# Optimization experiments

Measured on AMD Instinct MI355X. Metric: run time of the kernel, lower is better.

The kernel has to match this reference:

```python
import jax, jax.numpy as jnp
import numpy as np

LN_EPS = 1e-5

def _layernorm(x, g, b):
    mu = jnp.mean(x, axis=-1, keepdims=True)
    var = jnp.mean(jnp.square(x - mu), axis=-1, keepdims=True)
    return (x - mu) * jax.lax.rsqrt(var + LN_EPS) * g + b

def setup_inputs() -> dict:
    key = jax.random.key(0)
    ks = jax.random.split(key, 12)
    B, S, E = 8, 4096, 512
    H, DK = 64, 8          # d_k = E // H = 8 qubits per head
    NQ_FFN, FFN = 8, 2048
    TWO_PI = 2.0 * np.pi
    x = jax.random.normal(ks[0], (B, S, E), dtype=jnp.float32)
    # trainable RX phases per attention head/wire; trainable RY phases for FFN qubits
    theta_attn = jax.random.uniform(ks[1], (H, DK), dtype=jnp.float32, maxval=TWO_PI)
    theta_ffn = jax.random.uniform(ks[2], (NQ_FFN,), dtype=jnp.float32, maxval=TWO_PI)
    s_e = 1.0 / np.sqrt(E)
    W_comb = jax.random.uniform(ks[3], (E, E), dtype=jnp.float32, minval=-s_e, maxval=s_e)
    b_comb = jax.random.uniform(ks[4], (E,), dtype=jnp.float32, minval=-s_e, maxval=s_e)
    s_q = 1.0 / np.sqrt(NQ_FFN)
    W1 = jax.random.uniform(ks[5], (FFN, NQ_FFN), dtype=jnp.float32, minval=-s_q, maxval=s_q)
    b1 = jax.random.uniform(ks[6], (FFN,), dtype=jnp.float32, minval=-s_q, maxval=s_q)
    s_f = 1.0 / np.sqrt(FFN)
    W2 = jax.random.uniform(ks[7], (E, FFN), dtype=jnp.float32, minval=-s_f, maxval=s_f)
    b2 = jax.random.uniform(ks[8], (E,), dtype=jnp.float32, minval=-s_f, maxval=s_f)
    ln1_g = jnp.ones((E,), jnp.float32); ln1_b = jnp.zeros((E,), jnp.float32)
    ln2_g = jnp.ones((E,), jnp.float32); ln2_b = jnp.zeros((E,), jnp.float32)
    return {"x": x, "theta_attn": theta_attn, "W_comb": W_comb, "b_comb": b_comb,
            "ln1_g": ln1_g, "ln1_b": ln1_b, "theta_ffn": theta_ffn,
            "W1": W1, "b1": b1, "W2": W2, "b2": b2, "ln2_g": ln2_g, "ln2_b": ln2_b}

def reference(x, theta_attn, W_comb, b_comb, ln1_g, ln1_b, theta_ffn, W1, b1, W2, b2, ln2_g, ln2_b):
    B, S, E = x.shape
    H, DK = theta_attn.shape
    NQ = theta_ffn.shape[0]
    # Quantum attention heads: RX(x) then RX(theta) on |0> per wire -> <Z> = cos(x+theta)
    q = jnp.cos(x.reshape(B, S, H, DK) + theta_attn)  # [B,S,H,DK]
    attn_out = jnp.einsum('bse,fe->bsf', q.reshape(B, S, E), W_comb) + b_comb
    x1 = _layernorm(x + attn_out, ln1_g, ln1_b)
    # Quantum FFN layer: RY(x) then RY(theta) -> <Z> = cos(x+theta), first NQ features only
    fq = jnp.cos(x1[..., :NQ] + theta_ffn)            # [B,S,NQ]
    h = jax.nn.relu(jnp.einsum('bsq,fq->bsf', fq, W1) + b1)
    ffn_out = jnp.einsum('bsf,ef->bse', h, W2) + b2
    return _layernorm(x1 + ffn_out, ln2_g, ln2_b)
```

## Files before the change

kernel.cpp:

```cpp
#include <hip/hip_runtime.h>
#include <stdint.h>

typedef unsigned short u16;
typedef __bf16 bf16x8 __attribute__((ext_vector_type(8)));
typedef float f32x4 __attribute__((ext_vector_type(4)));

#define AS1(p) ((const __attribute__((address_space(1))) void*)(p))
#define AS3(p) ((__attribute__((address_space(3))) void*)(p))

__device__ __forceinline__ float b2f(u16 v){
    union { unsigned u; float f; } x; x.u = ((unsigned)v) << 16; return x.f;
}
__device__ __forceinline__ u16 f2b(float f){
    union { float f; unsigned u; } x; x.f = f;
    unsigned r = x.u + 0x7FFFu + ((x.u >> 16) & 1u);
    return (u16)(r >> 16);
}

__global__ __launch_bounds__(256) void probe_kernel(
    const u16* p0,const u16* p1,const u16* p2,const u16* p3,const u16* p4,
    const u16* p5,const u16* p6,const u16* p7,const u16* p8,const u16* p9,
    const u16* p10,const u16* p11,const u16* p12,
    int n0,int n1,int n2,int n3,int n4,int n5,int n6,int n7,int n8,int n9,
    int n10,int n11,int n12, int* flags)
{
    const u16* p; int n;
    switch (blockIdx.x) {
        case 0: p=p0; n=n0; break;   case 1: p=p1; n=n1; break;
        case 2: p=p2; n=n2; break;   case 3: p=p3; n=n3; break;
        case 4: p=p4; n=n4; break;   case 5: p=p5; n=n5; break;
        case 6: p=p6; n=n6; break;   case 7: p=p7; n=n7; break;
        case 8: p=p8; n=n8; break;   case 9: p=p9; n=n9; break;
        case 10: p=p10; n=n10; break; case 11: p=p11; n=n11; break;
        default: p=p12; n=n12; break;
    }
    int pairs = n >> 1; if (pairs > 2048) pairs = 2048;
    int strong = 0, znz = 0, tot = 0;
    for (int k = threadIdx.x; k < pairs; k += 256) {
        u16 lo = p[2*k], hi = p[2*k+1];
        int eh = (hi >> 7) & 0xFF;
        int el = (lo >> 7) & 0xFF;
        if (eh >= 0xF0 || (eh >= 1 && eh <= 0x40)) strong = 1;
        if (el >= 0xF0 || (el >= 1 && el <= 0x40)) strong = 1;
        if (lo == 0 && hi != 0) znz++;
        tot++;
    }
    __shared__ int ss, sz, st;
    if (threadIdx.x == 0) { ss = 0; sz = 0; st = 0; }
    __syncthreads();
    if (strong) atomicOr(&ss, 1);
    if (znz) atomicAdd(&sz, znz);
    atomicAdd(&st, tot);
    __syncthreads();
    if (threadIdx.x == 0) {
        flags[blockIdx.x] = (ss || (2 * sz > st)) ? 1 : 0;
        if (blockIdx.x == 0) flags[15] = 0;
    }
}

__global__ __launch_bounds__(256) void convert_kernel(
    const void* sWc, const void* sW2, const void* sW1,
    const void* sTa, const void* sBc, const void* sG1, const void* sB1l,
    const void* sTf, const void* sB1, const void* sB2, const void* sG2, const void* sB2l,
    u16* wbase, const int* flags)
{
    int b = blockIdx.x;
    const void* src; u16* dst; int n, fi, lb, tof32 = 0;
    if (b < 128)      { src=sWc; dst=wbase;          n=262144;  fi=2;  lb=b; }
    else if (b < 640) { src=sW2; dst=wbase+262144;   n=1048576; fi=9;  lb=b-128; }
    else if (b >= 643 && b < 651) { src=sW1; dst=wbase+1312256; n=16384; fi=7; lb=b-643; }
    else {
        lb = 0;
        switch (b) {
            case 640: src=sTa;  dst=wbase+1310720; n=512;  fi=1;  break;
            case 641: src=sBc;  dst=wbase+1311232; n=512;  fi=3;  break;
            case 642: src=sB2;  dst=wbase+1311744; n=512;  fi=10; break;
            case 651: src=sB1;  dst=wbase+1328640; n=2048; fi=8;  break;
            case 652: src=sG1;  dst=wbase+1330688; n=512;  fi=4;  break;
            case 653: src=sB1l; dst=wbase+1331200; n=512;  fi=5;  break;
            case 654: src=sG2;  dst=wbase+1331712; n=512;  fi=11; break;
            case 655: src=sB2l; dst=wbase+1332224; n=512;  fi=12; break;
            default:  src=sTf;  dst=wbase+1332736; n=8;    fi=6;  tof32=1; break;
        }
    }
    int i = lb * 256 + threadIdx.x;
    if (i * 8 >= n) return;
    if (tof32) {
        float* fd = (float*)dst;
        if (flags[fi]) {
            const float4* s = (const float4*)src;
            ((float4*)fd)[i*2] = s[i*2]; ((float4*)fd)[i*2+1] = s[i*2+1];
        } else {
            union { uint4 v; u16 h[8]; } sb;
            sb.v = ((const uint4*)src)[i];
            #pragma unroll
            for (int j = 0; j < 8; j++) fd[i*8+j] = b2f(sb.h[j]);
        }
        return;
    }
    if (flags[fi]) {
        const float4* s = (const float4*)src;
        float4 a = s[i*2], c = s[i*2+1];
        union { uint4 v; u16 h[8]; } o;
        o.h[0]=f2b(a.x); o.h[1]=f2b(a.y); o.h[2]=f2b(a.z); o.h[3]=f2b(a.w);
        o.h[4]=f2b(c.x); o.h[5]=f2b(c.y); o.h[6]=f2b(c.z); o.h[7]=f2b(c.w);
        ((uint4*)dst)[i] = o.v;
    } else {
        ((uint4*)dst)[i] = ((const uint4*)src)[i];
    }
}

__global__ __launch_bounds__(256) void qgen_kernel(
    const void* __restrict__ x, const u16* __restrict__ theta,
    u16* __restrict__ q, const int* flags)
{
    const int idx = blockIdx.x * 256 + threadIdx.x;
    const int col0 = (idx * 8) & 511;
    union { uint4 v; u16 h[8]; } tb;
    tb.v = *(const uint4*)(theta + col0);
    float xv[8];
    if (flags[0]) {
        const float4* p = (const float4*)x + idx * 2;
        float4 a = p[0], b = p[1];
        xv[0]=a.x; xv[1]=a.y; xv[2]=a.z; xv[3]=a.w;
        xv[4]=b.x; xv[5]=b.y; xv[6]=b.z; xv[7]=b.w;
    } else {
        union { uint4 v; u16 h[8]; } xb;
        xb.v = ((const uint4*)x)[idx];
        #pragma unroll
        for (int e = 0; e < 8; e++) xv[e] = b2f(xb.h[e]);
    }
    union { uint4 v; u16 h[8]; } o;
    #pragma unroll
    for (int e = 0; e < 8; e++) o.h[e] = f2b(__cosf(xv[e] + b2f(tb.h[e])));
    ((uint4*)q)[idx] = o.v;
}

__global__ __launch_bounds__(512, 2) void gemm1_fused(
    const u16* q, const void* __restrict__ x,
    const u16* __restrict__ Wt, const u16* __restrict__ bias,
    const u16* __restrict__ g1, const u16* __restrict__ b1l,
    const float* __restrict__ tf,
    u16* x1out, u16* __restrict__ fqout, const int* flags)
{
    __shared__ __align__(16) u16 As[2][128 * 64];
    __shared__ __align__(16) u16 Bs[2][512 * 64];
    const int K = 512, N = 512;
    const int tid  = threadIdx.x;
    const int lane = tid & 63;
    const int w    = tid >> 6;

    const int m0 = blockIdx.x * 128;

    const int srow = lane >> 3;
    const int scol = ((lane & 7) ^ srow) * 8;
    const int wm = (w >> 2) * 64;
    const int wn = (w & 3) * 128;
    const int fr   = lane & 15;
    const int quad = lane >> 4;
    const int fx   = fr & 7;
    const int isf32 = flags[0];

    f32x4 acc[4][8];
    #pragma unroll
    for (int i = 0; i < 4; i++)
        #pragma unroll
        for (int jj = 0; jj < 8; jj++)
            acc[i][jj] = f32x4{0.f, 0.f, 0.f, 0.f};

    const u16* Abase = q  + (size_t)m0 * K + scol;
    const u16* Bbase = Wt + scol;

    #pragma unroll
    for (int i = 0; i < 2; i++) {
        int c = w * 2 + i;
        int row = c * 8 + srow;
        __builtin_amdgcn_global_load_lds(AS1(Abase + (size_t)row * K),
                                         AS3(&As[0][c * 512]), 16, 0, 0);
    }
    #pragma unroll
    for (int i = 0; i < 8; i++) {
        int c = w * 8 + i;
        int row = c * 8 + srow;
        __builtin_amdgcn_global_load_lds(AS1(Bbase + (size_t)row * K),
                                         AS3(&Bs[0][c * 512]), 16, 0, 0);
    }

    int cur = 0;
    for (int kt = 0; kt < K; kt += 64) {
        __syncthreads();
        if (kt + 64 < K) {
            int nxt = cur ^ 1;
            #pragma unroll
            for (int i = 0; i < 2; i++) {
                int c = w * 2 + i;
                int row = c * 8 + srow;
                __builtin_amdgcn_global_load_lds(
                    AS1(Abase + (size_t)row * K + kt + 64),
                    AS3(&As[nxt][c * 512]), 16, 0, 0);
            }
            #pragma unroll
            for (int i = 0; i < 8; i++) {
                int c = w * 8 + i;
                int row = c * 8 + srow;
                __builtin_amdgcn_global_load_lds(
                    AS1(Bbase + (size_t)row * K + kt + 64),
                    AS3(&Bs[nxt][c * 512]), 16, 0, 0);
            }
        }
        #pragma unroll
        for (int kk = 0; kk < 2; kk++) {
            bf16x8 af[4];
            #pragma unroll
            for (int mi = 0; mi < 4; mi++)
                af[mi] = *(const bf16x8*)(&As[cur][(wm + mi * 16 + fr) * 64 +
                                          (((kk * 4 + quad) ^ fx) * 8)]);
            #pragma unroll
            for (int np = 0; np < 4; np++) {
                bf16x8 bfr[2];
                #pragma unroll
                for (int ni = 0; ni < 2; ni++)
                    bfr[ni] = *(const bf16x8*)(&Bs[cur][(wn + (np * 2 + ni) * 16 + fr) * 64 +
                                               (((kk * 4 + quad) ^ fx) * 8)]);
                #pragma unroll
                for (int mi = 0; mi < 4; mi++)
                    #pragma unroll
                    for (int ni = 0; ni < 2; ni++)
                        acc[mi][np * 2 + ni] = __builtin_amdgcn_mfma_f32_16x16x32_bf16(
                            af[mi], bfr[ni], acc[mi][np * 2 + ni], 0, 0, 0);
            }
        }
        cur ^= 1;
    }

    __syncthreads();
    u16* zt = &Bs[0][0];
    #pragma unroll
    for (int mi = 0; mi < 4; mi++) {
        #pragma unroll
        for (int nq = 0; nq < 8; nq++) {
            int n = wn + nq * 16 + fr;
            float bn = b2f(bias[n]);
            #pragma unroll
            for (int r = 0; r < 4; r++) {
                int lm = wm + mi * 16 + quad * 4 + r;
                float rv = isf32 ? ((const float*)x)[(size_t)(m0 + lm) * N + n]
                                 : b2f(((const u16*)x)[(size_t)(m0 + lm) * N + n]);
                zt[lm * 512 + n] = f2b(acc[mi][nq][r] + bn + rv);
            }
        }
    }
    __syncthreads();

    {
        union { uint4 v; u16 s[8]; } gb, bb;
        gb.v = *(const uint4*)(g1 + lane * 8);
        bb.v = *(const uint4*)(b1l + lane * 8);
        for (int i = 0; i < 16; i++) {
            int row = w * 16 + i;
            union { uint4 v; u16 s[8]; } zb;
            zb.v = ((const uint4*)(zt + row * 512))[lane];
            float xv[8], s = 0.f, ss = 0.f;
            #pragma unroll
            for (int jj = 0; jj < 8; jj++) {
                xv[jj] = b2f(zb.s[jj]); s += xv[jj]; ss += xv[jj] * xv[jj];
            }
            #pragma unroll
            for (int o = 32; o > 0; o >>= 1) { s += __shfl_down(s, o); ss += __shfl_down(ss, o); }
            s = __shfl(s, 0); ss = __shfl(ss, 0);
            float mu = s * (1.f / 512.f);
            float rs = rsqrtf(ss * (1.f / 512.f) - mu * mu + 1e-5f);
            float xn[8];
            union { uint4 v; u16 s[8]; } ob;
            #pragma unroll
            for (int jj = 0; jj < 8; jj++) {
                xn[jj] = (xv[jj] - mu) * rs * b2f(gb.s[jj]) + b2f(bb.s[jj]);
                ob.s[jj] = f2b(xn[jj]);
            }
            ((uint4*)(x1out + (size_t)(m0 + row) * 512))[lane] = ob.v;
            if (lane == 0) {
                #pragma unroll
                for (int jj = 0; jj < 8; jj++)
                    fqout[(size_t)(m0 + row) * 8 + jj] = f2b(__cosf(xn[jj] + tf[jj]));
            }
        }
    }
}

__global__ __launch_bounds__(512, 2) void gemm2_fused(
    const u16* __restrict__ fq, const u16* __restrict__ W1, const u16* __restrict__ b1,
    const u16* __restrict__ Wt, const u16* __restrict__ bias,
    const u16* __restrict__ res, const u16* __restrict__ g2, const u16* __restrict__ b2l,
    void* __restrict__ out, const int* flags)
{
    __shared__ __align__(16) u16 Bs[2][512 * 64];
    const int K = 2048, N = 512;
    const int tid  = threadIdx.x;
    const int lane = tid & 63;
    const int w    = tid >> 6;

    const int m0 = blockIdx.x * 128;

    const int srow = lane >> 3;
    const int scol = ((lane & 7) ^ srow) * 8;
    const int wm = (w >> 2) * 64;
    const int wn = (w & 3) * 128;
    const int fr   = lane & 15;
    const int quad = lane >> 4;
    const int fx   = fr & 7;
    const int isf32 = flags[0];

    bf16x8 fqf[4];
    #pragma unroll
    for (int mi = 0; mi < 4; mi++) {
        union { uint4 v; bf16x8 b; } z; z.v = uint4{0,0,0,0};
        if (quad == 0) z.v = *(const uint4*)(fq + (size_t)(m0 + wm + mi * 16 + fr) * 8);
        fqf[mi] = z.b;
    }

    const int krow = ((fr >> 2) * 8) + (fr & 3);

    union { uint4 v; bf16x8 b; } w1f[4];
    uint2 b1f[4];
    #pragma unroll
    for (int g = 0; g < 4; g++) {
        w1f[g].v = uint4{0,0,0,0};
        if (quad == 0)
            w1f[g].v = *(const uint4*)(W1 + (size_t)((g >> 1) * 32 + (g & 1) * 4 + krow) * 8);
        b1f[g] = *(const uint2*)(b1 + (g >> 1) * 32 + (g & 1) * 4 + quad * 8);
    }

    f32x4 acc[4][8];
    #pragma unroll
    for (int i = 0; i < 4; i++)
        #pragma unroll
        for (int jj = 0; jj < 8; jj++)
            acc[i][jj] = f32x4{0.f, 0.f, 0.f, 0.f};

    const u16* Bbase = Wt + scol;
    #pragma unroll
    for (int i = 0; i < 8; i++) {
        int c = w * 8 + i;
        int row = c * 8 + srow;
        __builtin_amdgcn_global_load_lds(AS1(Bbase + (size_t)row * K),
                                         AS3(&Bs[0][c * 512]), 16, 0, 0);
    }

    int cur = 0;
    for (int kt = 0; kt < K; kt += 64) {
        __syncthreads();
        if (kt + 64 < K) {
            int nxt = cur ^ 1;
            #pragma unroll
            for (int i = 0; i < 8; i++) {
                int c = w * 8 + i;
                int row = c * 8 + srow;
                __builtin_amdgcn_global_load_lds(
                    AS1(Bbase + (size_t)row * K + kt + 64),
                    AS3(&Bs[nxt][c * 512]), 16, 0, 0);
            }
        }
        #pragma unroll
        for (int kk = 0; kk < 2; kk++) {
            const u16* pb0 = (const u16*)&b1f[kk * 2 + 0];
            const u16* pb1 = (const u16*)&b1f[kk * 2 + 1];
            f32x4 c0 = {b2f(pb0[0]), b2f(pb0[1]), b2f(pb0[2]), b2f(pb0[3])};
            f32x4 c1 = {b2f(pb1[0]), b2f(pb1[1]), b2f(pb1[2]), b2f(pb1[3])};
            bf16x8 af[4];
            #pragma unroll
            for (int mi = 0; mi < 4; mi++) {
                f32x4 hv0 = __builtin_amdgcn_mfma_f32_16x16x32_bf16(
                    w1f[kk * 2 + 0].b, fqf[mi], c0, 0, 0, 0);
                f32x4 hv1 = __builtin_amdgcn_mfma_f32_16x16x32_bf16(
                    w1f[kk * 2 + 1].b, fqf[mi], c1, 0, 0, 0);
                #pragma unroll
                for (int r = 0; r < 4; r++) {
                    af[mi][r]     = (__bf16)fmaxf(hv0[r], 0.f);
                    af[mi][4 + r] = (__bf16)fmaxf(hv1[r], 0.f);
                }
            }
            #pragma unroll
            for (int np = 0; np < 4; np++) {
                bf16x8 bfr[2];
                #pragma unroll
                for (int ni = 0; ni < 2; ni++)
                    bfr[ni] = *(const bf16x8*)(&Bs[cur][(wn + (np * 2 + ni) * 16 + fr) * 64 +
                                               (((kk * 4 + quad) ^ fx) * 8)]);
                #pragma unroll
                for (int mi = 0; mi < 4; mi++)
                    #pragma unroll
                    for (int ni = 0; ni < 2; ni++)
                        acc[mi][np * 2 + ni] = __builtin_amdgcn_mfma_f32_16x16x32_bf16(
                            af[mi], bfr[ni], acc[mi][np * 2 + ni], 0, 0, 0);
            }
        }
        if (kt + 64 < K) {
            #pragma unroll
            for (int g = 0; g < 4; g++) {
                if (quad == 0)
                    w1f[g].v = *(const uint4*)(W1 +
                        (size_t)(kt + 64 + (g >> 1) * 32 + (g & 1) * 4 + krow) * 8);
                b1f[g] = *(const uint2*)(b1 + kt + 64 + (g >> 1) * 32 + (g & 1) * 4 + quad * 8);
            }
        }
        cur ^= 1;
    }

    __syncthreads();
    u16* zt = &Bs[0][0];
    #pragma unroll
    for (int mi = 0; mi < 4; mi++) {
        #pragma unroll
        for (int nq = 0; nq < 8; nq++) {
            int n = wn + nq * 16 + fr;
            float bn = b2f(bias[n]);
            #pragma unroll
            for (int r = 0; r < 4; r++) {
                int lm = wm + mi * 16 + quad * 4 + r;
                float v = acc[mi][nq][r] + bn + b2f(res[(size_t)(m0 + lm) * N + n]);
                zt[lm * 512 + n] = f2b(v);
            }
        }
    }
    __syncthreads();

    {
        union { uint4 v; u16 s[8]; } gb, bb;
        gb.v = *(const uint4*)(g2 + lane * 8);
        bb.v = *(const uint4*)(b2l + lane * 8);
        for (int i = 0; i < 16; i++) {
            int row = w * 16 + i;
            union { uint4 v; u16 s[8]; } zb;
            zb.v = ((const uint4*)(zt + row * 512))[lane];
            float xv[8], s = 0.f, ss = 0.f;
            #pragma unroll
            for (int jj = 0; jj < 8; jj++) {
                xv[jj] = b2f(zb.s[jj]); s += xv[jj]; ss += xv[jj] * xv[jj];
            }
            #pragma unroll
            for (int o = 32; o > 0; o >>= 1) { s += __shfl_down(s, o); ss += __shfl_down(ss, o); }
            s = __shfl(s, 0); ss = __shfl(ss, 0);
            float mu = s * (1.f / 512.f);
            float rs = rsqrtf(ss * (1.f / 512.f) - mu * mu + 1e-5f);
            size_t m = (size_t)(m0 + row);
            if (isf32) {
                float xn[8];
                #pragma unroll
                for (int jj = 0; jj < 8; jj++)
                    xn[jj] = (xv[jj] - mu) * rs * b2f(gb.s[jj]) + b2f(bb.s[jj]);
                float* po = (float*)out + m * N + lane * 8;
                *(float4*)po       = float4{xn[0], xn[1], xn[2], xn[3]};
                *(float4*)(po + 4) = float4{xn[4], xn[5], xn[6], xn[7]};
            } else {
                union { uint4 v; u16 s[8]; } ob;
                #pragma unroll
                for (int jj = 0; jj < 8; jj++)
                    ob.s[jj] = f2b((xv[jj] - mu) * rs * b2f(gb.s[jj]) + b2f(bb.s[jj]));
                ((uint4*)((u16*)out + m * N))[lane] = ob.v;
            }
        }
    }
}

extern "C" void kernel_launch(void* const* d_in, const int* in_sizes, int n_in,
                              void* d_out, int out_size, void* d_ws, size_t ws_size,
                              hipStream_t stream)
{
    u16* ws16 = (u16*)d_ws;
    u16* W     = ws16;
    int* flags = (int*)(ws16 + 1332752);
    u16* fq  = ws16 + 1332800;
    u16* x1  = ws16 + 1594944;
    u16* q   = x1;

    const u16*  wWc  = W;
    const u16*  wW2  = W + 262144;
    const u16*  wTa  = W + 1310720;
    const u16*  wBc  = W + 1311232;
    const u16*  wB2  = W + 1311744;
    const u16*  wW1  = W + 1312256;
    const u16*  wB1  = W + 1328640;
    const u16*  wG1  = W + 1330688;
    const u16*  wB1l = W + 1331200;
    const u16*  wG2  = W + 1331712;
    const u16*  wB2l = W + 1332224;
    const float* wTf = (const float*)(W + 1332736);

    probe_kernel<<<13, 256, 0, stream>>>(
        (const u16*)d_in[0], (const u16*)d_in[1], (const u16*)d_in[2],
        (const u16*)d_in[3], (const u16*)d_in[4], (const u16*)d_in[5],
        (const u16*)d_in[6], (const u16*)d_in[7], (const u16*)d_in[8],
        (const u16*)d_in[9], (const u16*)d_in[10], (const u16*)d_in[11],
        (const u16*)d_in[12],
        in_sizes[0], in_sizes[1], in_sizes[2], in_sizes[3], in_sizes[4],
        in_sizes[5], in_sizes[6], in_sizes[7], in_sizes[8], in_sizes[9],
        in_sizes[10], in_sizes[11], in_sizes[12], flags);

    convert_kernel<<<657, 256, 0, stream>>>(
        d_in[2], d_in[9], d_in[7], d_in[1], d_in[3], d_in[4], d_in[5],
        d_in[6], d_in[8], d_in[10], d_in[11], d_in[12], (u16*)W, flags);

    qgen_kernel<<<8192, 256, 0, stream>>>(d_in[0], wTa, q, flags);

    gemm1_fused<<<256, 512, 0, stream>>>(
        q, d_in[0], wWc, wBc, wG1, wB1l, wTf, x1, fq, flags);

    gemm2_fused<<<256, 512, 0, stream>>>(
        fq, wW1, wB1, wW2, wB2, x1, wG2, wB2l, d_out, flags);
}
```

Measured before the change: 301.3 us.

## Triple-buffer W2 tiles with K=32 stages and stage W1/b1 in LDS

Restructures the fused FFN GEMM main loop from double-buffered 64-wide K tiles to a three-stage ring of 32-wide K tiles, using explicit vmcnt waits so up to two tile loads stay in flight. W1 and b1 are preloaded into LDS once instead of being re-read from global memory every iteration, and s_setprio is raised around the MFMA section. This aims to hide global-load latency and cut per-iteration global traffic. In exchange there are twice as many barriers per K and LDS use grows to about 132 KB, which may lower occupancy compared with the intended two blocks per CU.

```diff
diff --git a/kernel.cpp b/kernel.cpp
--- a/kernel.cpp
+++ b/kernel.cpp
@@ -293,22 +293,22 @@
     const u16* __restrict__ res, const u16* __restrict__ g2, const u16* __restrict__ b2l,
     void* __restrict__ out, const int* flags)
 {
-    __shared__ __align__(16) u16 Bs[2][512 * 64];
-    const int K = 2048, N = 512;
+    __shared__ __align__(16) u16 pool[67584];
+    const int K = 2048, N = 512, NT = 64;
     const int tid  = threadIdx.x;
     const int lane = tid & 63;
     const int w    = tid >> 6;
 
     const int m0 = blockIdx.x * 128;
 
-    const int srow = lane >> 3;
-    const int scol = ((lane & 7) ^ srow) * 8;
     const int wm = (w >> 2) * 64;
     const int wn = (w & 3) * 128;
     const int fr   = lane & 15;
     const int quad = lane >> 4;
-    const int fx   = fr & 7;
     const int isf32 = flags[0];
+
+    u16* W1lds = pool + 49152;
+    u16* b1lds = pool + 65536;
 
     bf16x8 fqf[4];
     #pragma unroll
@@ -317,18 +317,7 @@
         if (quad == 0) z.v = *(const uint4*)(fq + (size_t)(m0 + wm + mi * 16 + fr) * 8);
         fqf[mi] = z.b;
     }
-
     const int krow = ((fr >> 2) * 8) + (fr & 3);
-
-    union { uint4 v; bf16x8 b; } w1f[4];
-    uint2 b1f[4];
-    #pragma unroll
-    for (int g = 0; g < 4; g++) {
-        w1f[g].v = uint4{0,0,0,0};
-        if (quad == 0)
-            w1f[g].v = *(const uint4*)(W1 + (size_t)((g >> 1) * 32 + (g & 1) * 4 + krow) * 8);
-        b1f[g] = *(const uint2*)(b1 + (g >> 1) * 32 + (g & 1) * 4 + quad * 8);
-    }
 
     f32x4 acc[4][8];
     #pragma unroll
@@ -337,77 +326,97 @@
         for (int jj = 0; jj < 8; jj++)
             acc[i][jj] = f32x4{0.f, 0.f, 0.f, 0.f};
 
-    const u16* Bbase = Wt + scol;
-    #pragma unroll
-    for (int i = 0; i < 8; i++) {
-        int c = w * 8 + i;
-        int row = c * 8 + srow;
-        __builtin_amdgcn_global_load_lds(AS1(Bbase + (size_t)row * K),
-                                         AS3(&Bs[0][c * 512]), 16, 0, 0);
-    }
-
-    int cur = 0;
-    for (int kt = 0; kt < K; kt += 64) {
-        __syncthreads();
-        if (kt + 64 < K) {
-            int nxt = cur ^ 1;
-            #pragma unroll
-            for (int i = 0; i < 8; i++) {
-                int c = w * 8 + i;
-                int row = c * 8 + srow;
-                __builtin_amdgcn_global_load_lds(
-                    AS1(Bbase + (size_t)row * K + kt + 64),
-                    AS3(&Bs[nxt][c * 512]), 16, 0, 0);
-            }
-        }
-        #pragma unroll
-        for (int kk = 0; kk < 2; kk++) {
-            const u16* pb0 = (const u16*)&b1f[kk * 2 + 0];
-            const u16* pb1 = (const u16*)&b1f[kk * 2 + 1];
-            f32x4 c0 = {b2f(pb0[0]), b2f(pb0[1]), b2f(pb0[2]), b2f(pb0[3])};
-            f32x4 c1 = {b2f(pb1[0]), b2f(pb1[1]), b2f(pb1[2]), b2f(pb1[3])};
-            bf16x8 af[4];
-            #pragma unroll
-            for (int mi = 0; mi < 4; mi++) {
-                f32x4 hv0 = __builtin_amdgcn_mfma_f32_16x16x32_bf16(
-                    w1f[kk * 2 + 0].b, fqf[mi], c0, 0, 0, 0);
-                f32x4 hv1 = __builtin_amdgcn_mfma_f32_16x16x32_bf16(
-                    w1f[kk * 2 + 1].b, fqf[mi], c1, 0, 0, 0);
-                #pragma unroll
-                for (int r = 0; r < 4; r++) {
-                    af[mi][r]     = (__bf16)fmaxf(hv0[r], 0.f);
-                    af[mi][4 + r] = (__bf16)fmaxf(hv1[r], 0.f);
-                }
-            }
-            #pragma unroll
-            for (int np = 0; np < 4; np++) {
-                bf16x8 bfr[2];
+    #pragma unroll
+    for (int i = 0; i < 4; i++) {
+        int c = w * 4 + i;
+        __builtin_amdgcn_global_load_lds(AS1(W1 + (size_t)c * 512 + lane * 8),
+                                         AS3(W1lds + c * 512), 16, 0, 0);
+    }
+    if (w < 4)
+        __builtin_amdgcn_global_load_lds(AS1(b1 + (size_t)w * 512 + lane * 8),
+                                         AS3(b1lds + w * 512), 16, 0, 0);
+    const int rr = lane >> 2;
+    const int soct = (lane & 3) ^ (rr & 3);
+    const u16* Bsrc = Wt + (size_t)rr * K + soct * 8;
+    auto STAGE = [&](int tt, int bb) {
+        #pragma unroll
+        for (int i = 0; i < 4; i++) {
+            int c = w * 4 + i;
+            __builtin_amdgcn_global_load_lds(
+                AS1(Bsrc + (size_t)(c * 16) * K + tt * 32),
+                AS3(pool + bb * 16384 + c * 512), 16, 0, 0);
+        }
+    };
+    STAGE(0, 0);
+    STAGE(1, 1);
+    __syncthreads();
+
+    union { uint4 v; bf16x8 b; } w1c0, w1c1;
+    uint2 b1c0, b1c1;
+    w1c0.v = uint4{0,0,0,0}; w1c1.v = uint4{0,0,0,0};
+    if (quad == 0) {
+        w1c0.v = *(const uint4*)(W1lds + (size_t)krow * 8);
+        w1c1.v = *(const uint4*)(W1lds + (size_t)(4 + krow) * 8);
+    }
+    b1c0 = *(const uint2*)(b1lds + quad * 8);
+    b1c1 = *(const uint2*)(b1lds + 4 + quad * 8);
+
+    const int rbase = (wn + fr) * 32 + ((quad ^ (fr & 3)) * 8);
+
+    int bcur = 0, bstage = 2;
+    for (int t = 0; t < NT; ++t) {
+        __builtin_amdgcn_sched_barrier(0);
+        if (t < NT - 1) asm volatile("s_waitcnt vmcnt(4)" ::: "memory");
+        else            asm volatile("s_waitcnt vmcnt(0)" ::: "memory");
+        __builtin_amdgcn_s_barrier();
+        __builtin_amdgcn_sched_barrier(0);
+        if (t + 2 < NT) STAGE(t + 2, bstage);
+
+        const u16* pb0 = (const u16*)&b1c0;
+        const u16* pb1 = (const u16*)&b1c1;
+        f32x4 c0 = {b2f(pb0[0]), b2f(pb0[1]), b2f(pb0[2]), b2f(pb0[3])};
+        f32x4 c1 = {b2f(pb1[0]), b2f(pb1[1]), b2f(pb1[2]), b2f(pb1[3])};
+        bf16x8 af[4];
+        #pragma unroll
+        for (int mi = 0; mi < 4; mi++) {
+            f32x4 hv0 = __builtin_amdgcn_mfma_f32_16x16x32_bf16(w1c0.b, fqf[mi], c0, 0, 0, 0);
+            f32x4 hv1 = __builtin_amdgcn_mfma_f32_16x16x32_bf16(w1c1.b, fqf[mi], c1, 0, 0, 0);
+            #pragma unroll
+            for (int r = 0; r < 4; r++) {
+                af[mi][r]     = (__bf16)fmaxf(hv0[r], 0.f);
+                af[mi][4 + r] = (__bf16)fmaxf(hv1[r], 0.f);
+            }
+        }
+        if (t + 1 < NT) {
+            if (quad == 0) {
+                w1c0.v = *(const uint4*)(W1lds + (size_t)((t + 1) * 32 + krow) * 8);
+                w1c1.v = *(const uint4*)(W1lds + (size_t)((t + 1) * 32 + 4 + krow) * 8);
+            }
+            b1c0 = *(const uint2*)(b1lds + (t + 1) * 32 + quad * 8);
+            b1c1 = *(const uint2*)(b1lds + (t + 1) * 32 + 4 + quad * 8);
+        }
+        const u16* BsBuf = pool + bcur * 16384;
+        __builtin_amdgcn_s_setprio(1);
+        #pragma unroll
+        for (int np = 0; np < 4; np++) {
+            bf16x8 bfr[2];
+            #pragma unroll
+            for (int ni = 0; ni < 2; ni++)
+                bfr[ni] = *(const bf16x8*)(BsBuf + rbase + (np * 2 + ni) * 512);
+            #pragma unroll
+            for (int mi = 0; mi < 4; mi++)
                 #pragma unroll
                 for (int ni = 0; ni < 2; ni++)
-                    bfr[ni] = *(const bf16x8*)(&Bs[cur][(wn + (np * 2 + ni) * 16 + fr) * 64 +
-                                               (((kk * 4 + quad) ^ fx) * 8)]);
-                #pragma unroll
-                for (int mi = 0; mi < 4; mi++)
-                    #pragma unroll
-                    for (int ni = 0; ni < 2; ni++)
-                        acc[mi][np * 2 + ni] = __builtin_amdgcn_mfma_f32_16x16x32_bf16(
-                            af[mi], bfr[ni], acc[mi][np * 2 + ni], 0, 0, 0);
-            }
-        }
-        if (kt + 64 < K) {
-            #pragma unroll
-            for (int g = 0; g < 4; g++) {
-                if (quad == 0)
-                    w1f[g].v = *(const uint4*)(W1 +
-                        (size_t)(kt + 64 + (g >> 1) * 32 + (g & 1) * 4 + krow) * 8);
-                b1f[g] = *(const uint2*)(b1 + kt + 64 + (g >> 1) * 32 + (g & 1) * 4 + quad * 8);
-            }
-        }
-        cur ^= 1;
-    }
-
-    __syncthreads();
-    u16* zt = &Bs[0][0];
+                    acc[mi][np * 2 + ni] = __builtin_amdgcn_mfma_f32_16x16x32_bf16(
+                        af[mi], bfr[ni], acc[mi][np * 2 + ni], 0, 0, 0);
+        }
+        __builtin_amdgcn_s_setprio(0);
+        bcur   = (bcur   == 2) ? 0 : bcur + 1;
+        bstage = (bstage == 2) ? 0 : bstage + 1;
+    }
+
+    __syncthreads();
+    u16* zt = pool;
     #pragma unroll
     for (int mi = 0; mi < 4; mi++) {
         #pragma unroll
```

Result: slower. 312.4 us (+3.7%).
